# Performance work log

Hardware: AMD Instinct MI355X
Metric: run time of the kernel (lower is better)

The kernel has to match this reference:

```python
import jax, jax.numpy as jnp
import numpy as np


def setup_inputs() -> dict:
    B, C, D = 8192, 2048, 1024
    key = jax.random.key(0)
    kx, kc = jax.random.split(key)
    x = jax.random.normal(kx, (B, D), dtype=jnp.float32)
    # kaiming_normal_ init for centers: std = sqrt(2 / fan_in) with fan_in = feat_dim
    centers = jax.random.normal(kc, (C, D), dtype=jnp.float32) * jnp.sqrt(2.0 / D)
    sigma = jnp.ones((C, D), dtype=jnp.float32)  # nn.init.ones_
    return {"x": x, "centers": centers, "sigma": sigma}


def reference(x, centers, sigma):
    # Original loop computes, per class i:
    #   dist[:, i] = diag(m @ diag(sigma[i]) @ m.T)  with m = x - centers[i]
    # which equals sum_d sigma[i,d] * (x[b,d] - centers[i,d])^2.
    # Expand the square to avoid the O(B*C*D) broadcast intermediate:
    #   dist[b,i] = (x^2) @ sigma[i] - 2 * x @ (sigma[i]*centers[i]) + sum_d sigma[i,d]*centers[i,d]^2
    xsq_term = jnp.einsum('bd,id->bi', x * x, sigma)            # [B, C]
    cross = jnp.einsum('bd,id->bi', x, sigma * centers)          # [B, C]
    const = jnp.sum(sigma * centers * centers, axis=-1)          # [C]
    dist = xsq_term - 2.0 * cross + const[None, :]
    return (centers, sigma, -dist)
```

## Files before the change

kernel.cpp:

```cpp
#include <hip/hip_runtime.h>
#include <hip/hip_bf16.h>


#define B_SZ 8192
#define C_SZ 2048
#define D_SZ 1024
#define K2   2048

typedef __attribute__((ext_vector_type(4))) float f32x4;
typedef __attribute__((ext_vector_type(8))) short bf16x8;

static __device__ __forceinline__ unsigned short f2bf(float f) {
  union { float f; unsigned int u; } v; v.f = f;
  unsigned int r = v.u + 0x7fffu + ((v.u >> 16) & 1u);
  return (unsigned short)(r >> 16);
}

__global__ __launch_bounds__(256) void prep(const float* __restrict__ x,
                                            const float* __restrict__ centers,
                                            const float* __restrict__ sigma,
                                            unsigned short* __restrict__ Aop,
                                            float* __restrict__ out_centers,
                                            float* __restrict__ out_sigma,
                                            unsigned short* __restrict__ Wop,
                                            float* __restrict__ cn) {
  if (blockIdx.x < 4096) {
    const long t = (long)blockIdx.x * 256 + threadIdx.x;
    const long e = t * 8;
    const long b = e >> 10;
    const int  d = (int)(e & 1023);
    const float4* xv = (const float4*)x;
    float4 v0 = xv[2 * t], v1 = xv[2 * t + 1];
    float vs[8] = {v0.x, v0.y, v0.z, v0.w, v1.x, v1.y, v1.z, v1.w};
    unsigned short sq[8] __attribute__((aligned(16)));
    unsigned short rw[8] __attribute__((aligned(16)));
#pragma unroll
    for (int j = 0; j < 8; ++j) {
      rw[j] = f2bf(vs[j]);
      sq[j] = f2bf(vs[j] * vs[j]);
    }
    *(uint4*)(Aop + b * K2 + d)        = *(uint4*)sq;
    *(uint4*)(Aop + b * K2 + D_SZ + d) = *(uint4*)rw;
  } else {
    const int grp = threadIdx.x >> 7;
    const int i = (blockIdx.x - 4096) * 2 + grp;
    const int t = threadIdx.x & 127;
    const long base = (long)i * D_SZ;
    const float4* cv = (const float4*)(centers + base);
    const float4* sv = (const float4*)(sigma + base);
    float4 c0 = cv[2 * t], c1 = cv[2 * t + 1];
    float4 s0 = sv[2 * t], s1 = sv[2 * t + 1];
    ((float4*)(out_centers + base))[2 * t]     = c0;
    ((float4*)(out_centers + base))[2 * t + 1] = c1;
    ((float4*)(out_sigma + base))[2 * t]       = s0;
    ((float4*)(out_sigma + base))[2 * t + 1]   = s1;
    float cs[8] = {c0.x, c0.y, c0.z, c0.w, c1.x, c1.y, c1.z, c1.w};
    float ss[8] = {s0.x, s0.y, s0.z, s0.w, s1.x, s1.y, s1.z, s1.w};
    unsigned short w1[8] __attribute__((aligned(16)));
    unsigned short w2[8] __attribute__((aligned(16)));
    float p = 0.0f;
#pragma unroll
    for (int j = 0; j < 8; ++j) {
      w1[j] = f2bf(-ss[j]);
      w2[j] = f2bf(2.0f * ss[j] * cs[j]);
      p += ss[j] * cs[j] * cs[j];
    }
    *(uint4*)(Wop + (long)i * K2 + t * 8)        = *(uint4*)w1;
    *(uint4*)(Wop + (long)i * K2 + D_SZ + t * 8) = *(uint4*)w2;
#pragma unroll
    for (int off = 32; off > 0; off >>= 1) p += __shfl_down(p, off, 64);
    __shared__ float red[2][2];
    if ((t & 63) == 0) red[grp][t >> 6] = p;
    __syncthreads();
    if (t == 0) cn[i] = -(red[grp][0] + red[grp][1]);
  }
}

#define VM6()  asm volatile("s_waitcnt vmcnt(6)" ::: "memory")
#define VM2()  asm volatile("s_waitcnt vmcnt(2)" ::: "memory")
#define VM0()  asm volatile("s_waitcnt vmcnt(0)" ::: "memory")
#define NOW()  ((void)0)
#define SB()   __builtin_amdgcn_sched_barrier(0)
#define BAR()  __builtin_amdgcn_s_barrier()

#define STAGE_A(C, KT)                                                          \
  do {                                                                          \
    __builtin_amdgcn_global_load_lds(                                           \
        (__attribute__((address_space(1))) void*)(aS + 0 * 64 * (long)K2 + (long)(KT) * 64), \
        (__attribute__((address_space(3))) void*)(&As[C][0 * 4096 + dstE]), 16, 0, 0);       \
    __builtin_amdgcn_global_load_lds(                                           \
        (__attribute__((address_space(1))) void*)(aS + 1 * 64 * (long)K2 + (long)(KT) * 64), \
        (__attribute__((address_space(3))) void*)(&As[C][1 * 4096 + dstE]), 16, 0, 0);       \
    __builtin_amdgcn_global_load_lds(                                           \
        (__attribute__((address_space(1))) void*)(aS + 2 * 64 * (long)K2 + (long)(KT) * 64), \
        (__attribute__((address_space(3))) void*)(&As[C][2 * 4096 + dstE]), 16, 0, 0);       \
    __builtin_amdgcn_global_load_lds(                                           \
        (__attribute__((address_space(1))) void*)(aS + 3 * 64 * (long)K2 + (long)(KT) * 64), \
        (__attribute__((address_space(3))) void*)(&As[C][3 * 4096 + dstE]), 16, 0, 0);       \
  } while (0)

#define STAGE_B(C, KT, KK)                                                      \
  do {                                                                          \
    __builtin_amdgcn_global_load_lds(                                           \
        (__attribute__((address_space(1))) void*)(bS + 0 * 128 * (long)K2 + (long)(KT) * 64 + (KK) * 32), \
        (__attribute__((address_space(3))) void*)(&Bs[C][0 * 4096 + dstE]), 16, 0, 0);                    \
    __builtin_amdgcn_global_load_lds(                                           \
        (__attribute__((address_space(1))) void*)(bS + 1 * 128 * (long)K2 + (long)(KT) * 64 + (KK) * 32), \
        (__attribute__((address_space(3))) void*)(&Bs[C][1 * 4096 + dstE]), 16, 0, 0);                    \
  } while (0)

#define LDA(BUF, KX, MI) (*(const bf16x8*)(&As[BUF][(aAddr ^ ((KX) * 32)) + (MI) * 1024]))
#define LDB(BUF, NI)     (*(const bf16x8*)(&Bs[BUF][bAddr + (NI) * 512]))

#define MM32(A0, A1, A2, A3, A4, A5, A6, A7, B0, B1, B2, B3)                     \
  acc[0][0] = __builtin_amdgcn_mfma_f32_16x16x32_bf16(A0, B0, acc[0][0], 0,0,0); \
  acc[0][1] = __builtin_amdgcn_mfma_f32_16x16x32_bf16(A0, B1, acc[0][1], 0,0,0); \
  acc[0][2] = __builtin_amdgcn_mfma_f32_16x16x32_bf16(A0, B2, acc[0][2], 0,0,0); \
  acc[0][3] = __builtin_amdgcn_mfma_f32_16x16x32_bf16(A0, B3, acc[0][3], 0,0,0); \
  acc[1][0] = __builtin_amdgcn_mfma_f32_16x16x32_bf16(A1, B0, acc[1][0], 0,0,0); \
  acc[1][1] = __builtin_amdgcn_mfma_f32_16x16x32_bf16(A1, B1, acc[1][1], 0,0,0); \
  acc[1][2] = __builtin_amdgcn_mfma_f32_16x16x32_bf16(A1, B2, acc[1][2], 0,0,0); \
  acc[1][3] = __builtin_amdgcn_mfma_f32_16x16x32_bf16(A1, B3, acc[1][3], 0,0,0); \
  acc[2][0] = __builtin_amdgcn_mfma_f32_16x16x32_bf16(A2, B0, acc[2][0], 0,0,0); \
  acc[2][1] = __builtin_amdgcn_mfma_f32_16x16x32_bf16(A2, B1, acc[2][1], 0,0,0); \
  acc[2][2] = __builtin_amdgcn_mfma_f32_16x16x32_bf16(A2, B2, acc[2][2], 0,0,0); \
  acc[2][3] = __builtin_amdgcn_mfma_f32_16x16x32_bf16(A2, B3, acc[2][3], 0,0,0); \
  acc[3][0] = __builtin_amdgcn_mfma_f32_16x16x32_bf16(A3, B0, acc[3][0], 0,0,0); \
  acc[3][1] = __builtin_amdgcn_mfma_f32_16x16x32_bf16(A3, B1, acc[3][1], 0,0,0); \
  acc[3][2] = __builtin_amdgcn_mfma_f32_16x16x32_bf16(A3, B2, acc[3][2], 0,0,0); \
  acc[3][3] = __builtin_amdgcn_mfma_f32_16x16x32_bf16(A3, B3, acc[3][3], 0,0,0); \
  acc[4][0] = __builtin_amdgcn_mfma_f32_16x16x32_bf16(A4, B0, acc[4][0], 0,0,0); \
  acc[4][1] = __builtin_amdgcn_mfma_f32_16x16x32_bf16(A4, B1, acc[4][1], 0,0,0); \
  acc[4][2] = __builtin_amdgcn_mfma_f32_16x16x32_bf16(A4, B2, acc[4][2], 0,0,0); \
  acc[4][3] = __builtin_amdgcn_mfma_f32_16x16x32_bf16(A4, B3, acc[4][3], 0,0,0); \
  acc[5][0] = __builtin_amdgcn_mfma_f32_16x16x32_bf16(A5, B0, acc[5][0], 0,0,0); \
  acc[5][1] = __builtin_amdgcn_mfma_f32_16x16x32_bf16(A5, B1, acc[5][1], 0,0,0); \
  acc[5][2] = __builtin_amdgcn_mfma_f32_16x16x32_bf16(A5, B2, acc[5][2], 0,0,0); \
  acc[5][3] = __builtin_amdgcn_mfma_f32_16x16x32_bf16(A5, B3, acc[5][3], 0,0,0); \
  acc[6][0] = __builtin_amdgcn_mfma_f32_16x16x32_bf16(A6, B0, acc[6][0], 0,0,0); \
  acc[6][1] = __builtin_amdgcn_mfma_f32_16x16x32_bf16(A6, B1, acc[6][1], 0,0,0); \
  acc[6][2] = __builtin_amdgcn_mfma_f32_16x16x32_bf16(A6, B2, acc[6][2], 0,0,0); \
  acc[6][3] = __builtin_amdgcn_mfma_f32_16x16x32_bf16(A6, B3, acc[6][3], 0,0,0); \
  acc[7][0] = __builtin_amdgcn_mfma_f32_16x16x32_bf16(A7, B0, acc[7][0], 0,0,0); \
  acc[7][1] = __builtin_amdgcn_mfma_f32_16x16x32_bf16(A7, B1, acc[7][1], 0,0,0); \
  acc[7][2] = __builtin_amdgcn_mfma_f32_16x16x32_bf16(A7, B2, acc[7][2], 0,0,0); \
  acc[7][3] = __builtin_amdgcn_mfma_f32_16x16x32_bf16(A7, B3, acc[7][3], 0,0,0);

#define TILE(AC, AN, AST, P1, P2, BS0, BS1, U, STGA, SB0_, SB1_, W0, W1, PRE)  \
  {                                                                   \
    if (SB0_) STAGE_B(BS0, (U) + 1, 1);                                        \
    if (STGA) STAGE_A(AST, (U) + 2);                                           \
    aQ0 = LDA(AC, 1, 0); aQ1 = LDA(AC, 1, 1);                                  \
    aQ2 = LDA(AC, 1, 2); aQ3 = LDA(AC, 1, 3);                                  \
    aQ4 = LDA(AC, 1, 4); aQ5 = LDA(AC, 1, 5);                                  \
    aQ6 = LDA(AC, 1, 6); aQ7 = LDA(AC, 1, 7);                                  \
    bQ0 = LDB(P1, 0); bQ1 = LDB(P1, 1); bQ2 = LDB(P1, 2); bQ3 = LDB(P1, 3);    \
    MM32(aP0, aP1, aP2, aP3, aP4, aP5, aP6, aP7, bP0, bP1, bP2, bP3)           \
    SB(); W0(); SB(); BAR();                                                   \
  }                                                                            \
  {                                                                   \
    if (SB1_) STAGE_B(BS1, (U) + 2, 0);                                        \
    if (PRE) {                                                                 \
      aP0 = LDA(AN, 0, 0); aP1 = LDA(AN, 0, 1);                                \
      aP2 = LDA(AN, 0, 2); aP3 = LDA(AN, 0, 3);                                \
      aP4 = LDA(AN, 0, 4); aP5 = LDA(AN, 0, 5);                                \
      aP6 = LDA(AN, 0, 6); aP7 = LDA(AN, 0, 7);                                \
      bP0 = LDB(P2, 0); bP1 = LDB(P2, 1); bP2 = LDB(P2, 2); bP3 = LDB(P2, 3);  \
    }                                                                          \
    MM32(aQ0, aQ1, aQ2, aQ3, aQ4, aQ5, aQ6, aQ7, bQ0, bQ1, bQ2, bQ3)          \
    SB(); W1(); SB(); BAR();                                                   \
  }

__global__ __launch_bounds__(512, 2) void gemm256(const unsigned short* __restrict__ A,
                                                  const unsigned short* __restrict__ W,
                                                  const float* __restrict__ cn,
                                                  float* __restrict__ out) {
  __shared__ __attribute__((aligned(16))) unsigned short As[3][16384];
  __shared__ __attribute__((aligned(16))) unsigned short Bs[3][8192];

  const int tid  = threadIdx.x;
  const int lane = tid & 63;
  const int wave = tid >> 6;
  const int wr = wave >> 2;
  const int wc = wave & 3;

  const int bid = blockIdx.x;
  const int xcd = bid & 7, idx = bid >> 3;
  const long rowBase = (long)(xcd * 4 + (idx >> 3)) * 256;
  const long colBase = (long)(idx & 7) * 256;

  const int sr = tid >> 3;
  const int sl = (tid & 7) ^ (sr & 7);
  const unsigned short* aS = A + (rowBase + sr) * (long)K2 + sl * 8;
  const int br = tid >> 2;
  const int bl = ((tid & 3) - (tid >> 3)) & 3;
  const unsigned short* bS = W + (colBase + br) * (long)K2 + bl * 8;
  const int dstE = tid * 8;

  const int l15 = lane & 15, l7 = lane & 7, q = lane >> 4;
  const int aAddr = (wr * 128 + l15) * 64 + ((q ^ l7) * 8);
  const int bAddr = (wc * 64 + l15) * 32 + (((q + (l15 >> 1)) & 3) * 8);

  f32x4 acc[8][4];
#pragma unroll
  for (int i = 0; i < 8; ++i)
#pragma unroll
    for (int j = 0; j < 4; ++j) acc[i][j] = (f32x4){0.f, 0.f, 0.f, 0.f};

  bf16x8 aP0, aP1, aP2, aP3, aP4, aP5, aP6, aP7;
  bf16x8 aQ0, aQ1, aQ2, aQ3, aQ4, aQ5, aQ6, aQ7;
  bf16x8 bP0, bP1, bP2, bP3, bQ0, bQ1, bQ2, bQ3;

  STAGE_A(0, 0);
  STAGE_B(0, 0, 0);
  STAGE_B(1, 0, 1);
  STAGE_A(1, 1);
  STAGE_B(2, 1, 0);
  VM6(); SB(); BAR();
  aP0 = LDA(0, 0, 0); aP1 = LDA(0, 0, 1); aP2 = LDA(0, 0, 2); aP3 = LDA(0, 0, 3);
  aP4 = LDA(0, 0, 4); aP5 = LDA(0, 0, 5); aP6 = LDA(0, 0, 6); aP7 = LDA(0, 0, 7);
  bP0 = LDB(0, 0); bP1 = LDB(0, 1); bP2 = LDB(0, 2); bP3 = LDB(0, 3);

#pragma unroll 1
  for (int u = 0; u < 30; u += 3) {
    TILE(0, 1, 2, 1, 2, 0, 1, u + 0, 1, 1, 1, VM6, VM6, 1);
    TILE(1, 2, 0, 0, 1, 2, 0, u + 1, 1, 1, 1, VM6, VM6, 1);
    TILE(2, 0, 1, 2, 0, 1, 2, u + 2, 1, 1, 1, VM6, VM6, 1);
  }
  TILE(0, 1, 2, 1, 2, 0, 1, 30, 0, 1, 0, VM2, VM0, 1);
  TILE(1, 2, 0, 0, 1, 2, 0, 31, 0, 0, 0, NOW, NOW, 0);

  const int crow = (lane >> 4) * 4;
  const int ccol = lane & 15;
#pragma unroll
  for (int ni = 0; ni < 4; ++ni) {
    const long col = colBase + wc * 64 + ni * 16 + ccol;
    const float c = cn[col];
#pragma unroll
    for (int mi = 0; mi < 8; ++mi) {
      const long row = rowBase + wr * 128 + mi * 16 + crow;
      float* o = out + row * C_SZ + col;
#pragma unroll
      for (int j = 0; j < 4; ++j) o[(long)j * C_SZ] = acc[mi][ni][j] + c;
    }
  }
}

extern "C" void kernel_launch(void* const* d_in, const int* in_sizes, int n_in,
                              void* d_out, int out_size, void* d_ws, size_t ws_size,
                              hipStream_t stream) {
  const float* x       = (const float*)d_in[0];
  const float* centers = (const float*)d_in[1];
  const float* sigma   = (const float*)d_in[2];
  float* out = (float*)d_out;

  unsigned short* Aop = (unsigned short*)d_ws;
  unsigned short* Wop = Aop + (long)B_SZ * K2;
  float* cnp = (float*)(Wop + (long)C_SZ * K2);

  prep<<<4096 + 1024, 256, 0, stream>>>(x, centers, sigma, Aop,
                                        out, out + (size_t)C_SZ * D_SZ, Wop, cnp);

  float* out2 = out + (size_t)2 * C_SZ * D_SZ;
  gemm256<<<256, 512, 0, stream>>>(Aop, Wop, cnp, out2);
}
```

Before: 83.58 us.

## Load B operand directly from global into registers, bypassing LDS

Removes the LDS staging buffers for the weight (B) operand. Each wave now loads its B fragments straight from global memory into registers one k-step ahead, and the vmcnt waits are retuned to match the new number of outstanding loads. This drops the LDS traffic and footprint spent on B, but B reads are no longer shared across the two wave rows, so global and L2 traffic go up. MFMA issue may also stall on global load latency.

```diff
diff --git a/kernel.cpp b/kernel.cpp
--- a/kernel.cpp
+++ b/kernel.cpp
@@ -76,9 +76,8 @@
   }
 }
 
-#define VM6()  asm volatile("s_waitcnt vmcnt(6)" ::: "memory")
-#define VM2()  asm volatile("s_waitcnt vmcnt(2)" ::: "memory")
-#define VM0()  asm volatile("s_waitcnt vmcnt(0)" ::: "memory")
+#define VM12() asm volatile("s_waitcnt vmcnt(12)" ::: "memory")
+#define VM8()  asm volatile("s_waitcnt vmcnt(8)" ::: "memory")
 #define NOW()  ((void)0)
 #define SB()   __builtin_amdgcn_sched_barrier(0)
 #define BAR()  __builtin_amdgcn_s_barrier()
@@ -99,18 +98,18 @@
         (__attribute__((address_space(3))) void*)(&As[C][3 * 4096 + dstE]), 16, 0, 0);       \
   } while (0)
 
-#define STAGE_B(C, KT, KK)                                                      \
-  do {                                                                          \
-    __builtin_amdgcn_global_load_lds(                                           \
-        (__attribute__((address_space(1))) void*)(bS + 0 * 128 * (long)K2 + (long)(KT) * 64 + (KK) * 32), \
-        (__attribute__((address_space(3))) void*)(&Bs[C][0 * 4096 + dstE]), 16, 0, 0);                    \
-    __builtin_amdgcn_global_load_lds(                                           \
-        (__attribute__((address_space(1))) void*)(bS + 1 * 128 * (long)K2 + (long)(KT) * 64 + (KK) * 32), \
-        (__attribute__((address_space(3))) void*)(&Bs[C][1 * 4096 + dstE]), 16, 0, 0);                    \
-  } while (0)
-
 #define LDA(BUF, KX, MI) (*(const bf16x8*)(&As[BUF][(aAddr ^ ((KX) * 32)) + (MI) * 1024]))
-#define LDB(BUF, NI)     (*(const bf16x8*)(&Bs[BUF][bAddr + (NI) * 512]))
+
+#define LOADB_P(T)                                                              \
+  bP0 = *(const bf16x8*)(bB0 + (long)(T) * 64);                                 \
+  bP1 = *(const bf16x8*)(bB1 + (long)(T) * 64);                                 \
+  bP2 = *(const bf16x8*)(bB2 + (long)(T) * 64);                                 \
+  bP3 = *(const bf16x8*)(bB3 + (long)(T) * 64);
+#define LOADB_Q(T)                                                              \
+  bQ0 = *(const bf16x8*)(bB0 + (long)(T) * 64 + 32);                            \
+  bQ1 = *(const bf16x8*)(bB1 + (long)(T) * 64 + 32);                            \
+  bQ2 = *(const bf16x8*)(bB2 + (long)(T) * 64 + 32);                            \
+  bQ3 = *(const bf16x8*)(bB3 + (long)(T) * 64 + 32);
 
 #define MM32(A0, A1, A2, A3, A4, A5, A6, A7, B0, B1, B2, B3)                     \
   acc[0][0] = __builtin_amdgcn_mfma_f32_16x16x32_bf16(A0, B0, acc[0][0], 0,0,0); \
@@ -146,29 +145,27 @@
   acc[7][2] = __builtin_amdgcn_mfma_f32_16x16x32_bf16(A7, B2, acc[7][2], 0,0,0); \
   acc[7][3] = __builtin_amdgcn_mfma_f32_16x16x32_bf16(A7, B3, acc[7][3], 0,0,0);
 
-#define TILE(AC, AN, AST, P1, P2, BS0, BS1, U, STGA, SB0_, SB1_, W0, W1, PRE)  \
+#define TILE(AC, AN, AST, U, STGA, LBQ, LBP, W0, PRE)                          \
   {                                                                   \
-    if (SB0_) STAGE_B(BS0, (U) + 1, 1);                                        \
+    if (LBQ) { LOADB_Q(U) }                                                    \
     if (STGA) STAGE_A(AST, (U) + 2);                                           \
     aQ0 = LDA(AC, 1, 0); aQ1 = LDA(AC, 1, 1);                                  \
     aQ2 = LDA(AC, 1, 2); aQ3 = LDA(AC, 1, 3);                                  \
     aQ4 = LDA(AC, 1, 4); aQ5 = LDA(AC, 1, 5);                                  \
     aQ6 = LDA(AC, 1, 6); aQ7 = LDA(AC, 1, 7);                                  \
-    bQ0 = LDB(P1, 0); bQ1 = LDB(P1, 1); bQ2 = LDB(P1, 2); bQ3 = LDB(P1, 3);    \
     MM32(aP0, aP1, aP2, aP3, aP4, aP5, aP6, aP7, bP0, bP1, bP2, bP3)           \
     SB(); W0(); SB(); BAR();                                                   \
   }                                                                            \
   {                                                                   \
-    if (SB1_) STAGE_B(BS1, (U) + 2, 0);                                        \
+    if (LBP) { LOADB_P((U) + 1) }                                              \
     if (PRE) {                                                                 \
       aP0 = LDA(AN, 0, 0); aP1 = LDA(AN, 0, 1);                                \
       aP2 = LDA(AN, 0, 2); aP3 = LDA(AN, 0, 3);                                \
       aP4 = LDA(AN, 0, 4); aP5 = LDA(AN, 0, 5);                                \
       aP6 = LDA(AN, 0, 6); aP7 = LDA(AN, 0, 7);                                \
-      bP0 = LDB(P2, 0); bP1 = LDB(P2, 1); bP2 = LDB(P2, 2); bP3 = LDB(P2, 3);  \
     }                                                                          \
     MM32(aQ0, aQ1, aQ2, aQ3, aQ4, aQ5, aQ6, aQ7, bQ0, bQ1, bQ2, bQ3)          \
-    SB(); W1(); SB(); BAR();                                                   \
+    SB(); BAR();                                                               \
   }
 
 __global__ __launch_bounds__(512, 2) void gemm256(const unsigned short* __restrict__ A,
@@ -176,7 +173,6 @@
                                                   const float* __restrict__ cn,
                                                   float* __restrict__ out) {
   __shared__ __attribute__((aligned(16))) unsigned short As[3][16384];
-  __shared__ __attribute__((aligned(16))) unsigned short Bs[3][8192];
 
   const int tid  = threadIdx.x;
   const int lane = tid & 63;
@@ -192,14 +188,15 @@
   const int sr = tid >> 3;
   const int sl = (tid & 7) ^ (sr & 7);
   const unsigned short* aS = A + (rowBase + sr) * (long)K2 + sl * 8;
-  const int br = tid >> 2;
-  const int bl = ((tid & 3) - (tid >> 3)) & 3;
-  const unsigned short* bS = W + (colBase + br) * (long)K2 + bl * 8;
   const int dstE = tid * 8;
 
   const int l15 = lane & 15, l7 = lane & 7, q = lane >> 4;
   const int aAddr = (wr * 128 + l15) * 64 + ((q ^ l7) * 8);
-  const int bAddr = (wc * 64 + l15) * 32 + (((q + (l15 >> 1)) & 3) * 8);
+
+  const unsigned short* bB0 = W + (colBase + wc * 64 +  0 + l15) * (long)K2 + q * 8;
+  const unsigned short* bB1 = W + (colBase + wc * 64 + 16 + l15) * (long)K2 + q * 8;
+  const unsigned short* bB2 = W + (colBase + wc * 64 + 32 + l15) * (long)K2 + q * 8;
+  const unsigned short* bB3 = W + (colBase + wc * 64 + 48 + l15) * (long)K2 + q * 8;
 
   f32x4 acc[8][4];
 #pragma unroll
@@ -212,23 +209,20 @@
   bf16x8 bP0, bP1, bP2, bP3, bQ0, bQ1, bQ2, bQ3;
 
   STAGE_A(0, 0);
-  STAGE_B(0, 0, 0);
-  STAGE_B(1, 0, 1);
   STAGE_A(1, 1);
-  STAGE_B(2, 1, 0);
-  VM6(); SB(); BAR();
+  LOADB_P(0)
+  VM8(); SB(); BAR();
   aP0 = LDA(0, 0, 0); aP1 = LDA(0, 0, 1); aP2 = LDA(0, 0, 2); aP3 = LDA(0, 0, 3);
   aP4 = LDA(0, 0, 4); aP5 = LDA(0, 0, 5); aP6 = LDA(0, 0, 6); aP7 = LDA(0, 0, 7);
-  bP0 = LDB(0, 0); bP1 = LDB(0, 1); bP2 = LDB(0, 2); bP3 = LDB(0, 3);
 
 #pragma unroll 1
   for (int u = 0; u < 30; u += 3) {
-    TILE(0, 1, 2, 1, 2, 0, 1, u + 0, 1, 1, 1, VM6, VM6, 1);
-    TILE(1, 2, 0, 0, 1, 2, 0, u + 1, 1, 1, 1, VM6, VM6, 1);
-    TILE(2, 0, 1, 2, 0, 1, 2, u + 2, 1, 1, 1, VM6, VM6, 1);
-  }
-  TILE(0, 1, 2, 1, 2, 0, 1, 30, 0, 1, 0, VM2, VM0, 1);
-  TILE(1, 2, 0, 0, 1, 2, 0, 31, 0, 0, 0, NOW, NOW, 0);
+    TILE(0, 1, 2, u + 0, 1, 1, 1, VM12, 1);
+    TILE(1, 2, 0, u + 1, 1, 1, 1, VM12, 1);
+    TILE(2, 0, 1, u + 2, 1, 1, 1, VM12, 1);
+  }
+  TILE(0, 1, 2, 30, 0, 1, 1, VM8, 1);
+  TILE(1, 2, 0, 31, 0, 1, 0, NOW, 0);
 
   const int crow = (lane >> 4) * 4;
   const int ccol = lane & 15;
```

Measured after the change: 113.3 us. +35.6%, slower.
